# Optimization experiments

Measured on AMD Instinct MI355X. Metric: run time of the kernel, lower is better.

## Reference

```python
import jax, jax.numpy as jnp
import numpy as np

# pywt db4 decomposition filters (dec_lo, dec_hi), length 8
_DEC_LO = np.array([-0.010597401784997278, 0.032883011666982945, 0.030841381835986965,
                    -0.18703481171888114, -0.02798376941698385, 0.6308807679295904,
                    0.7148465705525415, 0.23037781330885523], dtype=np.float32)
_DEC_HI = np.array([-0.23037781330885523, 0.7148465705525415, -0.6308807679295904,
                    -0.02798376941698385, 0.18703481171888114, 0.030841381835986965,
                    -0.032883011666982945, -0.010597401784997278], dtype=np.float32)
_L = 8  # filter length


def _dwt_single_level(a):
    """One level of pywt.dwt(a, 'db4', mode='symmetric') along last axis.
    a: [B, N] -> (cA, cD) each [B, (N+L-1)//2].
    pywt: symmetric-extend by L-1 each side, full-flip convolution, take [1::2].
    Equivalent: cross-correlate ext[:,1:] with reversed filter, stride 2, VALID."""
    ext = jnp.pad(a, ((0, 0), (_L - 1, _L - 1)), mode='symmetric')
    inp = ext[:, None, 1:]  # [B, 1, T-1]
    kern = jnp.stack([_DEC_LO[::-1].copy(), _DEC_HI[::-1].copy()])[:, None, :]  # [2,1,L]
    kern = jnp.asarray(kern, dtype=a.dtype)
    out = jax.lax.conv_general_dilated(inp, kern, window_strides=(2,), padding='VALID')  # [B,2,len]
    return out[:, 0, :], out[:, 1, :]


def _wavedec(x, level):
    """pywt.wavedec(x, 'db4', level=level, axis=-1): [cA_n, cD_n, ..., cD_1]."""
    a = x
    details = []
    for _ in range(level):
        a, d = _dwt_single_level(a)
        details.append(d)
    return [a] + details[::-1]


def setup_inputs() -> dict:
    key = jax.random.key(0)
    ks = jax.random.split(key, 6)
    B, IN, OUT = 4096, 4096, 4096
    inp = {"x": jax.random.normal(ks[0], (B, IN), dtype=jnp.float32)}
    for s in range(5):
        inp[f"basis{s}"] = jax.random.normal(ks[s + 1], (IN, OUT), dtype=jnp.float32)
    return inp


def reference(x, basis0, basis1, basis2, basis3, basis4):
    scales = 5
    coeffs = _wavedec(x, scales - 1)
    # original detaches x before the numpy DWT -> coeffs carry no grad to x
    coeffs = [jax.lax.stop_gradient(c) for c in coeffs]
    bases = [basis0, basis1, basis2, basis3, basis4]
    out = None
    for s in range(scales):
        c = coeffs[s]                       # [B, level_len]
        t = c @ bases[s][: c.shape[1], :]   # [B, OUT]
        out = t if out is None else out + t
    return out
```

## Files before the change

### kernel.cpp

```cpp
#include <hip/hip_runtime.h>
#include <stdint.h>


#define KPAD 4416

typedef __bf16 bf16x8 __attribute__((ext_vector_type(8)));
typedef float f32x4 __attribute__((ext_vector_type(4)));

__device__ __forceinline__ void split_bf(float v, unsigned short& h, unsigned short& l) {
  uint32_t u = __builtin_bit_cast(uint32_t, v);
  uint32_t hr = (u + 0x7FFFu + ((u >> 16) & 1u)) >> 16;
  h = (unsigned short)hr;
  float hf = __builtin_bit_cast(float, hr << 16);
  float d = v - hf;
  uint32_t du = __builtin_bit_cast(uint32_t, d);
  uint32_t lr = (du + 0x7FFFu + ((du >> 16) & 1u)) >> 16;
  l = (unsigned short)lr;
}

__global__ __launch_bounds__(256) void dwt_kernel(const float* __restrict__ x,
                                                  unsigned short* __restrict__ Ah,
                                                  unsigned short* __restrict__ Al) {
  __shared__ float bufA[4096];
  __shared__ float bufB[2052];
  const int tid = threadIdx.x;
  const int row = blockIdx.x;
  const size_t rowbase = (size_t)row * KPAD;

  {
    const float4* src = (const float4*)(x + (size_t)row * 4096);
    float4* dst = (float4*)bufA;
    for (int i = tid; i < 1024; i += 256) dst[i] = src[i];
  }
  __syncthreads();

  const float LOr[8] = {0.23037781330885523f, 0.7148465705525415f, 0.6308807679295904f,
                        -0.02798376941698385f, -0.18703481171888114f, 0.030841381835986965f,
                        0.032883011666982945f, -0.010597401784997278f};
  const float HIr[8] = {-0.010597401784997278f, -0.032883011666982945f, 0.030841381835986965f,
                        0.18703481171888114f, -0.02798376941698385f, -0.6308807679295904f,
                        0.7148465705525415f, -0.23037781330885523f};
  const int dOff[4] = {2304, 1216, 640, 320};

  float* cur = bufA;
  float* nxt = bufB;
  int N = 4096;
  for (int l = 0; l < 4; ++l) {
    const int M = (N + 7) >> 1;
    for (int t = tid; t < M; t += 256) {
      float lo = 0.f, hi = 0.f;
      const int base = 1 + 2 * t;
      #pragma unroll
      for (int j = 0; j < 8; ++j) {
        const int i = base + j;
        const int idx = (i < 7) ? (6 - i) : ((i < N + 7) ? (i - 7) : (2 * N + 6 - i));
        const float v = cur[idx];
        lo = fmaf(v, LOr[j], lo);
        hi = fmaf(v, HIr[j], hi);
      }
      unsigned short hh, hl;
      split_bf(hi, hh, hl);
      Ah[rowbase + dOff[l] + t] = hh;
      Al[rowbase + dOff[l] + t] = hl;
      if (l < 3) {
        nxt[t] = lo;
      } else {
        unsigned short ch, cl;
        split_bf(lo, ch, cl);
        Ah[rowbase + t] = ch;
        Al[rowbase + t] = cl;
      }
    }
    __syncthreads();
    float* tmp = cur; cur = nxt; nxt = tmp;
    N = M;
  }

  const int gs[5] = {262, 582, 1158, 2245, 4355};
  const int ge[5] = {320, 640, 1216, 2304, 4416};
  #pragma unroll
  for (int g = 0; g < 5; ++g)
    for (int i = gs[g] + tid; i < ge[g]; i += 256) {
      Ah[rowbase + i] = 0;
      Al[rowbase + i] = 0;
    }
}

__global__ __launch_bounds__(256) void bconv_kernel(const float* __restrict__ b0, const float* __restrict__ b1,
                                                    const float* __restrict__ b2, const float* __restrict__ b3,
                                                    const float* __restrict__ b4,
                                                    unsigned short* __restrict__ Bh,
                                                    unsigned short* __restrict__ Bl) {
  __shared__ float tile[64][65];
  const int tid = threadIdx.x;
  const int k0 = blockIdx.x * 64;
  const int n0 = blockIdx.y * 64;
  const int s = (k0 >= 2304) ? 4 : (k0 >= 1216) ? 3 : (k0 >= 640) ? 2 : (k0 >= 320) ? 1 : 0;
  const int offs[5] = {0, 320, 640, 1216, 2304};
  const int lens[5] = {262, 262, 518, 1029, 2051};
  const float* srcs[5] = {b0, b1, b2, b3, b4};
  const float* src = srcs[s];
  const int kl0 = k0 - offs[s];
  const int len = lens[s];

  #pragma unroll
  for (int r = 0; r < 4; ++r) {
    const int kr = r * 16 + (tid >> 4);
    const int nc = (tid & 15) * 4;
    const int kl = kl0 + kr;
    float4 v = make_float4(0.f, 0.f, 0.f, 0.f);
    if (kl < len) v = *(const float4*)(src + (size_t)kl * 4096 + n0 + nc);
    tile[kr][nc] = v.x; tile[kr][nc + 1] = v.y; tile[kr][nc + 2] = v.z; tile[kr][nc + 3] = v.w;
  }
  __syncthreads();

  const int nl = tid >> 2;
  const int kg = (tid & 3) * 16;
  uint4 hv[2]; uint4 lv[2];
  unsigned short* hb = (unsigned short*)hv;
  unsigned short* lb = (unsigned short*)lv;
  #pragma unroll
  for (int j = 0; j < 16; ++j) {
    unsigned short h, l;
    split_bf(tile[kg + j][nl], h, l);
    hb[j] = h; lb[j] = l;
  }
  const size_t dst = (size_t)(n0 + nl) * KPAD + (size_t)(k0 + kg);
  ((uint4*)(Bh + dst))[0] = hv[0];
  ((uint4*)(Bh + dst))[1] = hv[1];
  ((uint4*)(Bl + dst))[0] = lv[0];
  ((uint4*)(Bl + dst))[1] = lv[1];
}

#define GLD16(g, l)                                                                              \
  __builtin_amdgcn_global_load_lds((const __attribute__((address_space(1))) void*)(g),           \
                                   (__attribute__((address_space(3))) void*)(l), 16, 0, 0)

#define MFMA(a, b, c) __builtin_amdgcn_mfma_f32_16x16x32_bf16((a), (b), (c), 0, 0, 0)

__global__ __launch_bounds__(512, 2) void gemm_kernel(const unsigned short* __restrict__ Ah,
                                                      const unsigned short* __restrict__ Al,
                                                      const unsigned short* __restrict__ Bh,
                                                      const unsigned short* __restrict__ Bl,
                                                      float* __restrict__ C) {
  __shared__ __align__(16) char smem[131072];
  const int tid = threadIdx.x;
  const int wave = tid >> 6;
  const int lane = tid & 63;

  const int bid = blockIdx.x;
  const int wg = (bid & 7) * 32 + (bid >> 3);
  const int tm = wg >> 4, tn = wg & 15;
  const size_t bm0 = (size_t)tm * 256;
  const size_t bn0 = (size_t)tn * 256;
  const int wm = wave >> 2, wn = wave & 3;

  const int srow = tid >> 2;
  const int scs = (tid & 3) ^ (((srow >> 3) & 1) << 1);
  const size_t aoff = (bm0 + (size_t)srow) * KPAD + (size_t)scs * 8;
  const size_t boff = (bn0 + (size_t)srow) * KPAD + (size_t)scs * 8;
  const int wbase = wave * 1024;

#define STAGE_A(nb, kk)                                                   \
  do {                                                                    \
    char* lb = smem + (nb) * 65536 + wbase;                               \
    GLD16(Ah + aoff + (kk), lb);                                          \
    GLD16(Ah + aoff + 128 * KPAD + (kk), lb + 8192);                      \
    GLD16(Al + aoff + (kk), lb + 16384);                                  \
    GLD16(Al + aoff + 128 * KPAD + (kk), lb + 16384 + 8192);              \
  } while (0)
#define STAGE_B(nb, kk)                                                   \
  do {                                                                    \
    char* lb = smem + (nb) * 65536 + wbase;                               \
    GLD16(Bh + boff + (kk), lb + 32768);                                  \
    GLD16(Bh + boff + 128 * KPAD + (kk), lb + 32768 + 8192);              \
    GLD16(Bl + boff + (kk), lb + 49152);                                  \
    GLD16(Bl + boff + 128 * KPAD + (kk), lb + 49152 + 8192);              \
  } while (0)

  const int rsel = lane & 15;
  const int kswz = ((lane >> 4) * 16) ^ (((rsel >> 3) & 1) << 5);
  const int arb = (wm * 128 + rsel) * 64 + kswz;
  const int brb = (wn * 64 + rsel) * 64 + kswz;

  f32x4 acc[8][4] = {};

  STAGE_A(0, 0);
  STAGE_B(0, 0);
  asm volatile("s_waitcnt vmcnt(0)" ::: "memory");
  __builtin_amdgcn_s_barrier();

  const int NKT = KPAD / 32;
  for (int t = 0; t < NKT; ++t) {
    char* cb = smem + (t & 1) * 65536;
    const int nb = (t & 1) ^ 1;
    const bool st = (t + 1 < NKT);
    const size_t kn = (size_t)(t + 1) * 32;

    bf16x8 fbh[4], fbl[4];

    #pragma unroll
    for (int p = 0; p < 4; ++p) {
      if (p == 0) {
        #pragma unroll
        for (int q = 0; q < 4; ++q) {
          fbh[q] = *(const bf16x8*)(cb + 32768 + brb + q * 1024);
          fbl[q] = *(const bf16x8*)(cb + 49152 + brb + q * 1024);
        }
      }
      bf16x8 fah0 = *(const bf16x8*)(cb + arb + (2 * p) * 1024);
      bf16x8 fal0 = *(const bf16x8*)(cb + 16384 + arb + (2 * p) * 1024);
      bf16x8 fah1 = *(const bf16x8*)(cb + arb + (2 * p + 1) * 1024);
      bf16x8 fal1 = *(const bf16x8*)(cb + 16384 + arb + (2 * p + 1) * 1024);

      if (p == 0 && st) STAGE_A(nb, kn);
      if (p == 1 && st) STAGE_B(nb, kn);

      __builtin_amdgcn_s_barrier();
      __builtin_amdgcn_s_setprio(1);
      #pragma unroll
      for (int ni = 0; ni < 4; ++ni) {
        acc[2 * p][ni] = MFMA(fah0, fbh[ni], acc[2 * p][ni]);
        acc[2 * p][ni] = MFMA(fah0, fbl[ni], acc[2 * p][ni]);
        acc[2 * p][ni] = MFMA(fal0, fbh[ni], acc[2 * p][ni]);
        acc[2 * p + 1][ni] = MFMA(fah1, fbh[ni], acc[2 * p + 1][ni]);
        acc[2 * p + 1][ni] = MFMA(fah1, fbl[ni], acc[2 * p + 1][ni]);
        acc[2 * p + 1][ni] = MFMA(fal1, fbh[ni], acc[2 * p + 1][ni]);
      }
      __builtin_amdgcn_s_setprio(0);
      if (p == 3) asm volatile("s_waitcnt vmcnt(0)" ::: "memory");
      __builtin_amdgcn_s_barrier();
    }
  }

  const int col = lane & 15;
  const int rg = (lane >> 4) * 4;
  #pragma unroll
  for (int mi = 0; mi < 8; ++mi) {
    #pragma unroll
    for (int ni = 0; ni < 4; ++ni) {
      const size_t m = bm0 + (size_t)(wm * 128 + mi * 16 + rg);
      const size_t n = bn0 + (size_t)(wn * 64 + ni * 16 + col);
      float* cp = C + m * 4096 + n;
      #pragma unroll
      for (int rr = 0; rr < 4; ++rr) cp[(size_t)rr * 4096] = acc[mi][ni][rr];
    }
  }
}

extern "C" void kernel_launch(void* const* d_in, const int* in_sizes, int n_in,
                              void* d_out, int out_size, void* d_ws, size_t ws_size,
                              hipStream_t stream) {
  const float* x = (const float*)d_in[0];
  const float* b0 = (const float*)d_in[1];
  const float* b1 = (const float*)d_in[2];
  const float* b2 = (const float*)d_in[3];
  const float* b3 = (const float*)d_in[4];
  const float* b4 = (const float*)d_in[5];
  float* out = (float*)d_out;

  const size_t SA = (size_t)4096 * KPAD;
  unsigned short* Ah = (unsigned short*)d_ws;
  unsigned short* Al = Ah + SA;
  unsigned short* Bh = Al + SA;
  unsigned short* Bl = Bh + SA;

  dwt_kernel<<<4096, 256, 0, stream>>>(x, Ah, Al);
  bconv_kernel<<<dim3(KPAD / 64, 4096 / 64), 256, 0, stream>>>(b0, b1, b2, b3, b4, Bh, Bl);
  gemm_kernel<<<256, 512, 0, stream>>>(Ah, Al, Bh, Bl, out);
}
```

Measured before the change: 628.3 us.

## Switch GEMM to 32x32x16 MFMA and merge DWT and basis-conversion kernels

```diff
diff --git a/kernel.cpp b/kernel.cpp
--- a/kernel.cpp
+++ b/kernel.cpp
@@ -5,7 +5,7 @@
 #define KPAD 4416
 
 typedef __bf16 bf16x8 __attribute__((ext_vector_type(8)));
-typedef float f32x4 __attribute__((ext_vector_type(4)));
+typedef float f32x16 __attribute__((ext_vector_type(16)));
 
 __device__ __forceinline__ void split_bf(float v, unsigned short& h, unsigned short& l) {
   uint32_t u = __builtin_bit_cast(uint32_t, v);
@@ -18,125 +18,129 @@
   l = (unsigned short)lr;
 }
 
-__global__ __launch_bounds__(256) void dwt_kernel(const float* __restrict__ x,
-                                                  unsigned short* __restrict__ Ah,
-                                                  unsigned short* __restrict__ Al) {
-  __shared__ float bufA[4096];
-  __shared__ float bufB[2052];
+__global__ __launch_bounds__(256) void prep_kernel(const float* __restrict__ x,
+                                                   const float* __restrict__ b0, const float* __restrict__ b1,
+                                                   const float* __restrict__ b2, const float* __restrict__ b3,
+                                                   const float* __restrict__ b4,
+                                                   unsigned short* __restrict__ Ah,
+                                                   unsigned short* __restrict__ Al,
+                                                   unsigned short* __restrict__ Bh,
+                                                   unsigned short* __restrict__ Bl) {
+  __shared__ float smem[6148];
   const int tid = threadIdx.x;
-  const int row = blockIdx.x;
-  const size_t rowbase = (size_t)row * KPAD;
-
-  {
-    const float4* src = (const float4*)(x + (size_t)row * 4096);
-    float4* dst = (float4*)bufA;
-    for (int i = tid; i < 1024; i += 256) dst[i] = src[i];
+
+  if (blockIdx.x < 4096) {
+    float* bufA = smem;
+    float* bufB = smem + 4096;
+    const int row = blockIdx.x;
+    const size_t rowbase = (size_t)row * KPAD;
+
+    {
+      const float4* src = (const float4*)(x + (size_t)row * 4096);
+      float4* dst = (float4*)bufA;
+      for (int i = tid; i < 1024; i += 256) dst[i] = src[i];
+    }
+    __syncthreads();
+
+    const float LOr[8] = {0.23037781330885523f, 0.7148465705525415f, 0.6308807679295904f,
+                          -0.02798376941698385f, -0.18703481171888114f, 0.030841381835986965f,
+                          0.032883011666982945f, -0.010597401784997278f};
+    const float HIr[8] = {-0.010597401784997278f, -0.032883011666982945f, 0.030841381835986965f,
+                          0.18703481171888114f, -0.02798376941698385f, -0.6308807679295904f,
+                          0.7148465705525415f, -0.23037781330885523f};
+    const int dOff[4] = {2304, 1216, 640, 320};
+
+    float* cur = bufA;
+    float* nxt = bufB;
+    int N = 4096;
+    for (int l = 0; l < 4; ++l) {
+      const int M = (N + 7) >> 1;
+      for (int t = tid; t < M; t += 256) {
+        float lo = 0.f, hi = 0.f;
+        const int base = 1 + 2 * t;
+        #pragma unroll
+        for (int j = 0; j < 8; ++j) {
+          const int i = base + j;
+          const int idx = (i < 7) ? (6 - i) : ((i < N + 7) ? (i - 7) : (2 * N + 6 - i));
+          const float v = cur[idx];
+          lo = fmaf(v, LOr[j], lo);
+          hi = fmaf(v, HIr[j], hi);
+        }
+        unsigned short hh, hl;
+        split_bf(hi, hh, hl);
+        Ah[rowbase + dOff[l] + t] = hh;
+        Al[rowbase + dOff[l] + t] = hl;
+        if (l < 3) {
+          nxt[t] = lo;
+        } else {
+          unsigned short ch, cl;
+          split_bf(lo, ch, cl);
+          Ah[rowbase + t] = ch;
+          Al[rowbase + t] = cl;
+        }
+      }
+      __syncthreads();
+      float* tmp = cur; cur = nxt; nxt = tmp;
+      N = M;
+    }
+
+    const int gs[5] = {262, 582, 1158, 2245, 4355};
+    const int ge[5] = {320, 640, 1216, 2304, 4416};
+    #pragma unroll
+    for (int g = 0; g < 5; ++g)
+      for (int i = gs[g] + tid; i < ge[g]; i += 256) {
+        Ah[rowbase + i] = 0;
+        Al[rowbase + i] = 0;
+      }
+  } else {
+    float* tile = smem;
+    const int idx = blockIdx.x - 4096;
+    const int k0 = (idx % 69) * 64;
+    const int n0 = (idx / 69) * 64;
+    const int s = (k0 >= 2304) ? 4 : (k0 >= 1216) ? 3 : (k0 >= 640) ? 2 : (k0 >= 320) ? 1 : 0;
+    const int offs[5] = {0, 320, 640, 1216, 2304};
+    const int lens[5] = {262, 262, 518, 1029, 2051};
+    const float* srcs[5] = {b0, b1, b2, b3, b4};
+    const float* src = srcs[s];
+    const int kl0 = k0 - offs[s];
+    const int len = lens[s];
+
+    #pragma unroll
+    for (int r = 0; r < 4; ++r) {
+      const int kr = r * 16 + (tid >> 4);
+      const int nc = (tid & 15) * 4;
+      const int kl = kl0 + kr;
+      float4 v = make_float4(0.f, 0.f, 0.f, 0.f);
+      if (kl < len) v = *(const float4*)(src + (size_t)kl * 4096 + n0 + nc);
+      tile[kr * 65 + nc] = v.x; tile[kr * 65 + nc + 1] = v.y;
+      tile[kr * 65 + nc + 2] = v.z; tile[kr * 65 + nc + 3] = v.w;
+    }
+    __syncthreads();
+
+    const int nl = tid >> 2;
+    const int kg = (tid & 3) * 16;
+    uint4 hv[2]; uint4 lv[2];
+    unsigned short* hb = (unsigned short*)hv;
+    unsigned short* lb = (unsigned short*)lv;
+    #pragma unroll
+    for (int j = 0; j < 16; ++j) {
+      unsigned short h, l;
+      split_bf(tile[(kg + j) * 65 + nl], h, l);
+      hb[j] = h; lb[j] = l;
+    }
+    const size_t dst = (size_t)(n0 + nl) * KPAD + (size_t)(k0 + kg);
+    ((uint4*)(Bh + dst))[0] = hv[0];
+    ((uint4*)(Bh + dst))[1] = hv[1];
+    ((uint4*)(Bl + dst))[0] = lv[0];
+    ((uint4*)(Bl + dst))[1] = lv[1];
   }
-  __syncthreads();
-
-  const float LOr[8] = {0.23037781330885523f, 0.7148465705525415f, 0.6308807679295904f,
-                        -0.02798376941698385f, -0.18703481171888114f, 0.030841381835986965f,
-                        0.032883011666982945f, -0.010597401784997278f};
-  const float HIr[8] = {-0.010597401784997278f, -0.032883011666982945f, 0.030841381835986965f,
-                        0.18703481171888114f, -0.02798376941698385f, -0.6308807679295904f,
-                        0.7148465705525415f, -0.23037781330885523f};
-  const int dOff[4] = {2304, 1216, 640, 320};
-
-  float* cur = bufA;
-  float* nxt = bufB;
-  int N = 4096;
-  for (int l = 0; l < 4; ++l) {
-    const int M = (N + 7) >> 1;
-    for (int t = tid; t < M; t += 256) {
-      float lo = 0.f, hi = 0.f;
-      const int base = 1 + 2 * t;
-      #pragma unroll
-      for (int j = 0; j < 8; ++j) {
-        const int i = base + j;
-        const int idx = (i < 7) ? (6 - i) : ((i < N + 7) ? (i - 7) : (2 * N + 6 - i));
-        const float v = cur[idx];
-        lo = fmaf(v, LOr[j], lo);
-        hi = fmaf(v, HIr[j], hi);
-      }
-      unsigned short hh, hl;
-      split_bf(hi, hh, hl);
-      Ah[rowbase + dOff[l] + t] = hh;
-      Al[rowbase + dOff[l] + t] = hl;
-      if (l < 3) {
-        nxt[t] = lo;
-      } else {
-        unsigned short ch, cl;
-        split_bf(lo, ch, cl);
-        Ah[rowbase + t] = ch;
-        Al[rowbase + t] = cl;
-      }
-    }
-    __syncthreads();
-    float* tmp = cur; cur = nxt; nxt = tmp;
-    N = M;
-  }
-
-  const int gs[5] = {262, 582, 1158, 2245, 4355};
-  const int ge[5] = {320, 640, 1216, 2304, 4416};
-  #pragma unroll
-  for (int g = 0; g < 5; ++g)
-    for (int i = gs[g] + tid; i < ge[g]; i += 256) {
-      Ah[rowbase + i] = 0;
-      Al[rowbase + i] = 0;
-    }
-}
-
-__global__ __launch_bounds__(256) void bconv_kernel(const float* __restrict__ b0, const float* __restrict__ b1,
-                                                    const float* __restrict__ b2, const float* __restrict__ b3,
-                                                    const float* __restrict__ b4,
-                                                    unsigned short* __restrict__ Bh,
-                                                    unsigned short* __restrict__ Bl) {
-  __shared__ float tile[64][65];
-  const int tid = threadIdx.x;
-  const int k0 = blockIdx.x * 64;
-  const int n0 = blockIdx.y * 64;
-  const int s = (k0 >= 2304) ? 4 : (k0 >= 1216) ? 3 : (k0 >= 640) ? 2 : (k0 >= 320) ? 1 : 0;
-  const int offs[5] = {0, 320, 640, 1216, 2304};
-  const int lens[5] = {262, 262, 518, 1029, 2051};
-  const float* srcs[5] = {b0, b1, b2, b3, b4};
-  const float* src = srcs[s];
-  const int kl0 = k0 - offs[s];
-  const int len = lens[s];
-
-  #pragma unroll
-  for (int r = 0; r < 4; ++r) {
-    const int kr = r * 16 + (tid >> 4);
-    const int nc = (tid & 15) * 4;
-    const int kl = kl0 + kr;
-    float4 v = make_float4(0.f, 0.f, 0.f, 0.f);
-    if (kl < len) v = *(const float4*)(src + (size_t)kl * 4096 + n0 + nc);
-    tile[kr][nc] = v.x; tile[kr][nc + 1] = v.y; tile[kr][nc + 2] = v.z; tile[kr][nc + 3] = v.w;
-  }
-  __syncthreads();
-
-  const int nl = tid >> 2;
-  const int kg = (tid & 3) * 16;
-  uint4 hv[2]; uint4 lv[2];
-  unsigned short* hb = (unsigned short*)hv;
-  unsigned short* lb = (unsigned short*)lv;
-  #pragma unroll
-  for (int j = 0; j < 16; ++j) {
-    unsigned short h, l;
-    split_bf(tile[kg + j][nl], h, l);
-    hb[j] = h; lb[j] = l;
-  }
-  const size_t dst = (size_t)(n0 + nl) * KPAD + (size_t)(k0 + kg);
-  ((uint4*)(Bh + dst))[0] = hv[0];
-  ((uint4*)(Bh + dst))[1] = hv[1];
-  ((uint4*)(Bl + dst))[0] = lv[0];
-  ((uint4*)(Bl + dst))[1] = lv[1];
 }
 
 #define GLD16(g, l)                                                                              \
   __builtin_amdgcn_global_load_lds((const __attribute__((address_space(1))) void*)(g),           \
                                    (__attribute__((address_space(3))) void*)(l), 16, 0, 0)
 
-#define MFMA(a, b, c) __builtin_amdgcn_mfma_f32_16x16x32_bf16((a), (b), (c), 0, 0, 0)
+#define MFMA32(a, b, c) __builtin_amdgcn_mfma_f32_32x32x16_bf16((a), (b), (c), 0, 0, 0)
 
 __global__ __launch_bounds__(512, 2) void gemm_kernel(const unsigned short* __restrict__ Ah,
                                                       const unsigned short* __restrict__ Al,
@@ -178,12 +182,12 @@
     GLD16(Bl + boff + 128 * KPAD + (kk), lb + 49152 + 8192);              \
   } while (0)
 
-  const int rsel = lane & 15;
-  const int kswz = ((lane >> 4) * 16) ^ (((rsel >> 3) & 1) << 5);
-  const int arb = (wm * 128 + rsel) * 64 + kswz;
-  const int brb = (wn * 64 + rsel) * 64 + kswz;
-
-  f32x4 acc[8][4] = {};
+  const int r31 = lane & 31;
+  const int kc0 = ((lane >> 5) << 4) | ((r31 & 8) << 2);
+  const int abase = (wm * 128 + r31) * 64;
+  const int bbase = (wn * 64 + r31) * 64;
+
+  f32x16 acc[4][2] = {};
 
   STAGE_A(0, 0);
   STAGE_B(0, 0);
@@ -197,21 +201,24 @@
     const bool st = (t + 1 < NKT);
     const size_t kn = (size_t)(t + 1) * 32;
 
-    bf16x8 fbh[4], fbl[4];
+    bf16x8 fbh[2][2], fbl[2][2];
 
     #pragma unroll
     for (int p = 0; p < 4; ++p) {
       if (p == 0) {
         #pragma unroll
-        for (int q = 0; q < 4; ++q) {
-          fbh[q] = *(const bf16x8*)(cb + 32768 + brb + q * 1024);
-          fbl[q] = *(const bf16x8*)(cb + 49152 + brb + q * 1024);
+        for (int ni = 0; ni < 2; ++ni) {
+          #pragma unroll
+          for (int kk = 0; kk < 2; ++kk) {
+            fbh[ni][kk] = *(const bf16x8*)(cb + 32768 + bbase + ni * 2048 + (kc0 ^ (kk << 5)));
+            fbl[ni][kk] = *(const bf16x8*)(cb + 49152 + bbase + ni * 2048 + (kc0 ^ (kk << 5)));
+          }
         }
       }
-      bf16x8 fah0 = *(const bf16x8*)(cb + arb + (2 * p) * 1024);
-      bf16x8 fal0 = *(const bf16x8*)(cb + 16384 + arb + (2 * p) * 1024);
-      bf16x8 fah1 = *(const bf16x8*)(cb + arb + (2 * p + 1) * 1024);
-      bf16x8 fal1 = *(const bf16x8*)(cb + 16384 + arb + (2 * p + 1) * 1024);
+      bf16x8 fah0 = *(const bf16x8*)(cb + abase + p * 2048 + kc0);
+      bf16x8 fah1 = *(const bf16x8*)(cb + abase + p * 2048 + (kc0 ^ 32));
+      bf16x8 fal0 = *(const bf16x8*)(cb + 16384 + abase + p * 2048 + kc0);
+      bf16x8 fal1 = *(const bf16x8*)(cb + 16384 + abase + p * 2048 + (kc0 ^ 32));
 
       if (p == 0 && st) STAGE_A(nb, kn);
       if (p == 1 && st) STAGE_B(nb, kn);
@@ -219,31 +226,36 @@
       __builtin_amdgcn_s_barrier();
       __builtin_amdgcn_s_setprio(1);
       #pragma unroll
-      for (int ni = 0; ni < 4; ++ni) {
-        acc[2 * p][ni] = MFMA(fah0, fbh[ni], acc[2 * p][ni]);
-        acc[2 * p][ni] = MFMA(fah0, fbl[ni], acc[2 * p][ni]);
-        acc[2 * p][ni] = MFMA(fal0, fbh[ni], acc[2 * p][ni]);
-        acc[2 * p + 1][ni] = MFMA(fah1, fbh[ni], acc[2 * p + 1][ni]);
-        acc[2 * p + 1][ni] = MFMA(fah1, fbl[ni], acc[2 * p + 1][ni]);
-        acc[2 * p + 1][ni] = MFMA(fal1, fbh[ni], acc[2 * p + 1][ni]);
-      }
+      for (int ni = 0; ni < 2; ++ni) acc[p][ni] = MFMA32(fah0, fbh[ni][0], acc[p][ni]);
+      #pragma unroll
+      for (int ni = 0; ni < 2; ++ni) acc[p][ni] = MFMA32(fal0, fbh[ni][0], acc[p][ni]);
+      #pragma unroll
+      for (int ni = 0; ni < 2; ++ni) acc[p][ni] = MFMA32(fah0, fbl[ni][0], acc[p][ni]);
+      #pragma unroll
+      for (int ni = 0; ni < 2; ++ni) acc[p][ni] = MFMA32(fah1, fbh[ni][1], acc[p][ni]);
+      #pragma unroll
+      for (int ni = 0; ni < 2; ++ni) acc[p][ni] = MFMA32(fal1, fbh[ni][1], acc[p][ni]);
+      #pragma unroll
+      for (int ni = 0; ni < 2; ++ni) acc[p][ni] = MFMA32(fah1, fbl[ni][1], acc[p][ni]);
       __builtin_amdgcn_s_setprio(0);
       if (p == 3) asm volatile("s_waitcnt vmcnt(0)" ::: "memory");
       __builtin_amdgcn_s_barrier();
     }
   }
 
-  const int col = lane & 15;
-  const int rg = (lane >> 4) * 4;
+  const int col = lane & 31;
+  const int rhi = (lane >> 5) * 4;
   #pragma unroll
-  for (int mi = 0; mi < 8; ++mi) {
-    #pragma unroll
-    for (int ni = 0; ni < 4; ++ni) {
-      const size_t m = bm0 + (size_t)(wm * 128 + mi * 16 + rg);
-      const size_t n = bn0 + (size_t)(wn * 64 + ni * 16 + col);
-      float* cp = C + m * 4096 + n;
-      #pragma unroll
-      for (int rr = 0; rr < 4; ++rr) cp[(size_t)rr * 4096] = acc[mi][ni][rr];
+  for (int mi = 0; mi < 4; ++mi) {
+    #pragma unroll
+    for (int ni = 0; ni < 2; ++ni) {
+      const size_t m0 = bm0 + (size_t)(wm * 128 + mi * 32);
+      const size_t n = bn0 + (size_t)(wn * 64 + ni * 32 + col);
+      #pragma unroll
+      for (int reg = 0; reg < 16; ++reg) {
+        const int row = (reg & 3) + 8 * (reg >> 2) + rhi;
+        C[(m0 + row) * 4096 + n] = acc[mi][ni][reg];
+      }
     }
   }
 }
@@ -265,7 +277,6 @@
   unsigned short* Bh = Al + SA;
   unsigned short* Bl = Bh + SA;
 
-  dwt_kernel<<<4096, 256, 0, stream>>>(x, Ah, Al);
-  bconv_kernel<<<dim3(KPAD / 64, 4096 / 64), 256, 0, stream>>>(b0, b1, b2, b3, b4, Bh, Bl);
+  prep_kernel<<<4096 + 4416, 256, 0, stream>>>(x, b0, b1, b2, b3, b4, Ah, Al, Bh, Bl);
   gemm_kernel<<<256, 512, 0, stream>>>(Ah, Al, Bh, Bl, out);
 }
```

Measured after the change: 674.4 us. 7.4% more time.
